# Optimization experiments

Measured on AMD Instinct MI355X. Metric: run time of the kernel, lower is better.

Reference implementation:

```python
import jax, jax.numpy as jnp
import numpy as np

H = 2048        # hidden_nodes
T = 8192        # timeseries length
WASHOUT = 200
SPECTRAL_RADIUS = 0.9


def setup_inputs() -> dict:
    key = jax.random.key(0)
    k1, k2, k3 = jax.random.split(key, 3)
    u = jax.random.normal(k1, (T,), dtype=jnp.float32)
    # w_res ~ uniform(-0.5, 0.5), rescaled to approximate spectral radius 0.9
    w_res = jax.random.uniform(k2, (H, H), dtype=jnp.float32) - 0.5
    unif_std = 1.0 / np.sqrt(12.0)
    w_res = w_res * np.float32(SPECTRAL_RADIUS / (unif_std * np.sqrt(H)))
    # w_in ~ uniform(-0.5, 0.5) * input_scaling(=1.0)
    w_in = jax.random.uniform(k3, (H,), dtype=jnp.float32) - 0.5
    w_out = jnp.ones((H,), dtype=jnp.float32)
    # w_out_density = 1.0 -> mask covers all nodes (identity gather)
    w_out_mask = jnp.arange(H, dtype=jnp.int32)
    return {"u": u, "w_res": w_res, "w_in": w_in, "w_out": w_out,
            "w_out_mask": w_out_mask, "washout": WASHOUT}


def reference(u, w_res, w_in, w_out, w_out_mask, washout):
    # Inference path (y=None, awgn_test_std=0, adc_quantization=None):
    #   x_{t} = tanh(w_in * u_t + w_res @ x_{t-1}); X[t] = x_t[mask]
    #   return X[washout:] @ w_out
    def step(x, u_t):
        x = jnp.tanh(w_in * u_t + w_res @ x)   # [H]
        return x, x[w_out_mask]                # carry, per-step readout row

    x0 = jnp.zeros((w_res.shape[0],), dtype=u.dtype)
    _, X = jax.lax.scan(step, x0, u)           # X: [T, output_dim]
    return X[washout:] @ w_out                 # [T - washout]
```

## Files before the change

### kernel.cpp

```cpp
#include <hip/hip_runtime.h>
#include <math.h>


#define H_   2048
#define RPB  8
#define NBLK 256
typedef unsigned long long ull;

__global__ void esn_zero(float* __restrict__ p, int n)
{
    int i = blockIdx.x * blockDim.x + threadIdx.x;
    int stride = gridDim.x * blockDim.x;
    for (; i < n; i += stride) p[i] = 0.0f;
}

__global__ __launch_bounds__(1024) void esn_scatter_c(const int* __restrict__ mask,
                                                      const float* __restrict__ w_out,
                                                      float* __restrict__ ws_f, int H)
{
    float* c = ws_f + 8192;
    for (int i = threadIdx.x; i < H; i += blockDim.x)
        atomicAdd(&c[mask[i]], w_out[i]);
}

__global__ __launch_bounds__(256) void esn_run(const float* __restrict__ u,
                                               const float* __restrict__ w_res,
                                               const float* __restrict__ w_in,
                                               float* __restrict__ out,
                                               float* __restrict__ ws_f,
                                               int T, int washout, int use_part)
{
    __shared__ float Wlds[RPB * H_];
    __shared__ float xs[H_];
    __shared__ float psum[4];

    const int tid  = threadIdx.x;
    const int wave = tid >> 6;
    const int lane = tid & 63;
    const int bid  = blockIdx.x;
    const int r0 = 2 * wave;
    const int grow0 = bid * RPB + r0;

    {
        const float4* src = (const float4*)(w_res + (size_t)bid * RPB * H_);
        float4* dst = (float4*)Wlds;
        for (int i = tid; i < RPB * H_ / 4; i += 256) dst[i] = src[i];
    }
    float win_l = 0.f, c_l = 0.f;
    if (lane < 2) {
        win_l = w_in[grow0 + lane];
        c_l   = ws_f[8192 + grow0 + lane];
    }

    ull* pairs = (ull*)ws_f;
    float* part = ws_f + 10240;

    const float4* w0p = (const float4*)(Wlds + (r0)     * H_);
    const float4* w1p = (const float4*)(Wlds + (r0 + 1) * H_);
    const float4* xs4 = (const float4*)xs;

    float u_next = u[0];
    __syncthreads();

    for (int k = 0; k < T; ++k) {
        const ull* sp = pairs + (k & 1) * H_;
        ull*       dp = pairs + ((k + 1) & 1) * H_;
        float uk = u_next;
        if (k + 1 < T) u_next = u[k + 1];

        ull pv[8];
#pragma unroll
        for (int i = 0; i < 8; ++i)
            pv[i] = __hip_atomic_load(sp + (i << 8) + tid, __ATOMIC_RELAXED,
                                      __HIP_MEMORY_SCOPE_AGENT);

        float4 a0 = {0.f,0.f,0.f,0.f}, a1 = {0.f,0.f,0.f,0.f};
#pragma unroll
        for (int c = 0; c < 8; ++c) {
            int spins = 0;
            while ((unsigned)(pv[c] >> 32) != (unsigned)k) {
                pv[c] = __hip_atomic_load(sp + (c << 8) + tid, __ATOMIC_RELAXED,
                                          __HIP_MEMORY_SCOPE_AGENT);
                if (++spins > 2000000) break;
            }
            xs[(c << 8) + tid] = __uint_as_float((unsigned)pv[c]);
            __syncthreads();
            float4 xv  = xs4[(c << 6) + lane];
            float4 wv0 = w0p[(c << 6) + lane];
            float4 wv1 = w1p[(c << 6) + lane];
            a0.x = fmaf(wv0.x, xv.x, a0.x); a0.y = fmaf(wv0.y, xv.y, a0.y);
            a0.z = fmaf(wv0.z, xv.z, a0.z); a0.w = fmaf(wv0.w, xv.w, a0.w);
            a1.x = fmaf(wv1.x, xv.x, a1.x); a1.y = fmaf(wv1.y, xv.y, a1.y);
            a1.z = fmaf(wv1.z, xv.z, a1.z); a1.w = fmaf(wv1.w, xv.w, a1.w);
        }
        float s0 = (a0.x + a0.y) + (a0.z + a0.w);
        float s1 = (a1.x + a1.y) + (a1.z + a1.w);
#pragma unroll
        for (int d = 1; d < 64; d <<= 1) {
            s0 += __shfl_xor(s0, d);
            s1 += __shfl_xor(s1, d);
        }

        if (lane < 2) {
            float z = fmaf(win_l, uk, (lane == 0) ? s0 : s1);
            z = fminf(fmaxf(z, -15.f), 15.f);
            float e = __expf(2.f * z);
            float t = (e - 1.f) / (e + 1.f);
            ull p = ((ull)(unsigned)(k + 1) << 32) | (ull)__float_as_uint(t);
            (void)__hip_atomic_exchange(dp + grow0 + lane, p, __ATOMIC_RELAXED,
                                        __HIP_MEMORY_SCOPE_AGENT);
            float pr = c_l * t;
            pr += __shfl_xor(pr, 1);
            if (lane == 0) psum[wave] = pr;
        }
        __syncthreads();

        if (tid == 0) {
            float pw = (psum[0] + psum[1]) + (psum[2] + psum[3]);
            if (use_part) part[(size_t)k * NBLK + bid] = pw;
            else if (k >= washout) atomicAdd(&out[k - washout], pw);
        }
    }
}

__global__ __launch_bounds__(256) void esn_reduce(const float* __restrict__ part,
                                                  float* __restrict__ out,
                                                  int out_size, int washout)
{
    int wv = threadIdx.x >> 6, lane = threadIdx.x & 63;
    int t = blockIdx.x * 4 + wv;
    if (t >= out_size) return;
    const float4* p = (const float4*)(part + (size_t)(t + washout) * NBLK);
    float4 v = p[lane];
    float s = (v.x + v.y) + (v.z + v.w);
#pragma unroll
    for (int d = 1; d < 64; d <<= 1) s += __shfl_xor(s, d);
    if (lane == 0) out[t] = s;
}

extern "C" void kernel_launch(void* const* d_in, const int* in_sizes, int n_in,
                              void* d_out, int out_size, void* d_ws, size_t ws_size,
                              hipStream_t stream)
{
    const float* u     = (const float*)d_in[0];
    const float* w_res = (const float*)d_in[1];
    const float* w_in  = (const float*)d_in[2];
    const float* w_out = (const float*)d_in[3];
    const int*   mask  = (const int*)d_in[4];
    int T = in_sizes[0];
    int H = in_sizes[2];
    int washout = T - out_size;
    float* out  = (float*)d_out;
    float* ws_f = (float*)d_ws;

    size_t need = (size_t)(10240 + (size_t)T * NBLK) * 4;
    int use_part = (ws_size >= need) ? 1 : 0;

    hipLaunchKernelGGL(esn_zero, dim3(64), dim3(256), 0, stream, ws_f, 10240);
    if (!use_part)
        hipLaunchKernelGGL(esn_zero, dim3(32), dim3(256), 0, stream, out, out_size);
    hipLaunchKernelGGL(esn_scatter_c, dim3(1), dim3(1024), 0, stream, mask, w_out, ws_f, H);

    void* args[] = { (void*)&u, (void*)&w_res, (void*)&w_in, (void*)&out,
                     (void*)&ws_f, (void*)&T, (void*)&washout, (void*)&use_part };
    hipError_t e = hipLaunchCooperativeKernel((const void*)esn_run,
                                              dim3(NBLK), dim3(256),
                                              args, 0, stream);
    if (e != hipSuccess) {
        hipLaunchKernelGGL(esn_run, dim3(NBLK), dim3(256), 0, stream,
                           u, w_res, w_in, out, ws_f, T, washout, use_part);
    }
    if (use_part)
        hipLaunchKernelGGL(esn_reduce, dim3((out_size + 3) / 4), dim3(256), 0, stream,
                           ws_f + 10240, out, out_size, washout);
}
```

Baseline: 38.02 ms.

## Split matvec by columns per wave, drop per-chunk block barriers, batch spin polls

Each wave now owns a 512-column slice of x and computes partial dot products for all 8 rows of the block, reading x straight from the polled registers instead of staging it in shared memory. This removes the eight __syncthreads per timestep that followed each chunk, leaving a single barrier to combine the per-wave partials through a double-buffered shared array. The spin wait now polls all eight chunks together with two outstanding loads per chunk, and the published value uses an atomic store instead of an exchange. In exchange, each wave does eight cross-lane reductions instead of two, and one wave handles the tanh, the publish and the readout.

Measured after the change: 42.77 ms. 12.5% more time.

```diff
diff --git a/kernel.cpp b/kernel.cpp
--- a/kernel.cpp
+++ b/kernel.cpp
@@ -31,15 +31,14 @@
                                                int T, int washout, int use_part)
 {
     __shared__ float Wlds[RPB * H_];
-    __shared__ float xs[H_];
-    __shared__ float psum[4];
+    __shared__ float psum[2][4][RPB];
 
     const int tid  = threadIdx.x;
     const int wave = tid >> 6;
     const int lane = tid & 63;
     const int bid  = blockIdx.x;
-    const int r0 = 2 * wave;
-    const int grow0 = bid * RPB + r0;
+    const int grow = bid * RPB;
+    const int jbase = (wave << 9) + lane;
 
     {
         const float4* src = (const float4*)(w_res + (size_t)bid * RPB * H_);
@@ -47,78 +46,97 @@
         for (int i = tid; i < RPB * H_ / 4; i += 256) dst[i] = src[i];
     }
     float win_l = 0.f, c_l = 0.f;
-    if (lane < 2) {
-        win_l = w_in[grow0 + lane];
-        c_l   = ws_f[8192 + grow0 + lane];
+    if (wave == 0 && lane < RPB) {
+        win_l = w_in[grow + lane];
+        c_l   = ws_f[8192 + grow + lane];
     }
 
     ull* pairs = (ull*)ws_f;
     float* part = ws_f + 10240;
 
-    const float4* w0p = (const float4*)(Wlds + (r0)     * H_);
-    const float4* w1p = (const float4*)(Wlds + (r0 + 1) * H_);
-    const float4* xs4 = (const float4*)xs;
-
     float u_next = u[0];
     __syncthreads();
 
     for (int k = 0; k < T; ++k) {
-        const ull* sp = pairs + (k & 1) * H_;
+        const ull* sp = pairs + (k & 1) * H_ + jbase;
         ull*       dp = pairs + ((k + 1) & 1) * H_;
         float uk = u_next;
         if (k + 1 < T) u_next = u[k + 1];
 
-        ull pv[8];
+        ull a[8], b[8];
 #pragma unroll
-        for (int i = 0; i < 8; ++i)
-            pv[i] = __hip_atomic_load(sp + (i << 8) + tid, __ATOMIC_RELAXED,
-                                      __HIP_MEMORY_SCOPE_AGENT);
+        for (int c = 0; c < 8; ++c)
+            a[c] = __hip_atomic_load(sp + (c << 6), __ATOMIC_RELAXED,
+                                     __HIP_MEMORY_SCOPE_AGENT);
+#pragma unroll
+        for (int c = 0; c < 8; ++c)
+            b[c] = __hip_atomic_load(sp + (c << 6), __ATOMIC_RELAXED,
+                                     __HIP_MEMORY_SCOPE_AGENT);
+        {
+            int spins = 0;
+            for (;;) {
+                unsigned stale = 0;
+#pragma unroll
+                for (int c = 0; c < 8; ++c) {
+                    if ((unsigned)(a[c] >> 32) != (unsigned)k) {
+                        a[c] = b[c];
+                        b[c] = __hip_atomic_load(sp + (c << 6), __ATOMIC_RELAXED,
+                                                 __HIP_MEMORY_SCOPE_AGENT);
+                        stale = 1;
+                    }
+                }
+                if (!stale) break;
+                if (++spins > 1000000) break;
+            }
+        }
 
         float4 a0 = {0.f,0.f,0.f,0.f}, a1 = {0.f,0.f,0.f,0.f};
 #pragma unroll
         for (int c = 0; c < 8; ++c) {
-            int spins = 0;
-            while ((unsigned)(pv[c] >> 32) != (unsigned)k) {
-                pv[c] = __hip_atomic_load(sp + (c << 8) + tid, __ATOMIC_RELAXED,
-                                          __HIP_MEMORY_SCOPE_AGENT);
-                if (++spins > 2000000) break;
-            }
-            xs[(c << 8) + tid] = __uint_as_float((unsigned)pv[c]);
-            __syncthreads();
-            float4 xv  = xs4[(c << 6) + lane];
-            float4 wv0 = w0p[(c << 6) + lane];
-            float4 wv1 = w1p[(c << 6) + lane];
-            a0.x = fmaf(wv0.x, xv.x, a0.x); a0.y = fmaf(wv0.y, xv.y, a0.y);
-            a0.z = fmaf(wv0.z, xv.z, a0.z); a0.w = fmaf(wv0.w, xv.w, a0.w);
-            a1.x = fmaf(wv1.x, xv.x, a1.x); a1.y = fmaf(wv1.y, xv.y, a1.y);
-            a1.z = fmaf(wv1.z, xv.z, a1.z); a1.w = fmaf(wv1.w, xv.w, a1.w);
+            float xv = __uint_as_float((unsigned)a[c]);
+            const float* wp = Wlds + (c << 6) + jbase;
+            a0.x = fmaf(wp[0 * H_], xv, a0.x);
+            a0.y = fmaf(wp[1 * H_], xv, a0.y);
+            a0.z = fmaf(wp[2 * H_], xv, a0.z);
+            a0.w = fmaf(wp[3 * H_], xv, a0.w);
+            a1.x = fmaf(wp[4 * H_], xv, a1.x);
+            a1.y = fmaf(wp[5 * H_], xv, a1.y);
+            a1.z = fmaf(wp[6 * H_], xv, a1.z);
+            a1.w = fmaf(wp[7 * H_], xv, a1.w);
         }
-        float s0 = (a0.x + a0.y) + (a0.z + a0.w);
-        float s1 = (a1.x + a1.y) + (a1.z + a1.w);
 #pragma unroll
         for (int d = 1; d < 64; d <<= 1) {
-            s0 += __shfl_xor(s0, d);
-            s1 += __shfl_xor(s1, d);
+            a0.x += __shfl_xor(a0.x, d); a0.y += __shfl_xor(a0.y, d);
+            a0.z += __shfl_xor(a0.z, d); a0.w += __shfl_xor(a0.w, d);
+            a1.x += __shfl_xor(a1.x, d); a1.y += __shfl_xor(a1.y, d);
+            a1.z += __shfl_xor(a1.z, d); a1.w += __shfl_xor(a1.w, d);
         }
+        if (lane == 0) {
+            float* ps = psum[k & 1][wave];
+            ps[0] = a0.x; ps[1] = a0.y; ps[2] = a0.z; ps[3] = a0.w;
+            ps[4] = a1.x; ps[5] = a1.y; ps[6] = a1.z; ps[7] = a1.w;
+        }
+        __syncthreads();
 
-        if (lane < 2) {
-            float z = fmaf(win_l, uk, (lane == 0) ? s0 : s1);
+        if (wave == 0 && lane < RPB) {
+            const int p = k & 1;
+            float z = (psum[p][0][lane] + psum[p][1][lane]) +
+                      (psum[p][2][lane] + psum[p][3][lane]);
+            z = fmaf(win_l, uk, z);
             z = fminf(fmaxf(z, -15.f), 15.f);
             float e = __expf(2.f * z);
             float t = (e - 1.f) / (e + 1.f);
-            ull p = ((ull)(unsigned)(k + 1) << 32) | (ull)__float_as_uint(t);
-            (void)__hip_atomic_exchange(dp + grow0 + lane, p, __ATOMIC_RELAXED,
-                                        __HIP_MEMORY_SCOPE_AGENT);
-            float pr = c_l * t;
-            pr += __shfl_xor(pr, 1);
-            if (lane == 0) psum[wave] = pr;
-        }
-        __syncthreads();
-
-        if (tid == 0) {
-            float pw = (psum[0] + psum[1]) + (psum[2] + psum[3]);
-            if (use_part) part[(size_t)k * NBLK + bid] = pw;
-            else if (k >= washout) atomicAdd(&out[k - washout], pw);
+            ull pr = ((ull)(unsigned)(k + 1) << 32) | (ull)__float_as_uint(t);
+            __hip_atomic_store(dp + grow + lane, pr, __ATOMIC_RELAXED,
+                               __HIP_MEMORY_SCOPE_AGENT);
+            float po = c_l * t;
+            po += __shfl_xor(po, 1);
+            po += __shfl_xor(po, 2);
+            po += __shfl_xor(po, 4);
+            if (lane == 0) {
+                if (use_part) part[(size_t)k * NBLK + bid] = po;
+                else if (k >= washout) atomicAdd(&out[k - washout], po);
+            }
         }
     }
 }
```

## Poll all state chunks together and drop per-chunk and epilogue barriers

Applied to the files above, without the earlier changes.

Each thread now issues two rounds of relaxed atomic loads for all eight chunks of the previous state and keeps polling only the stale ones. When all chunks are fresh it writes them to LDS behind a single raw s_barrier, replacing the eight __syncthreads calls that followed each chunk's spin. The per-block partial sum no longer goes through a shared psum and a trailing __syncthreads. Each wave atomically adds its two-row contribution into the partial buffer, which now has to be zeroed by an extra launch. This cuts barrier count per timestep on the serial recurrence path, at the cost of more atomic traffic and a larger zeroing pass.

New measurement: 34.35 ms. 1.11x faster.

```diff
diff --git a/kernel.cpp b/kernel.cpp
--- a/kernel.cpp
+++ b/kernel.cpp
@@ -32,14 +32,13 @@
 {
     __shared__ float Wlds[RPB * H_];
     __shared__ float xs[H_];
-    __shared__ float psum[4];
 
     const int tid  = threadIdx.x;
     const int wave = tid >> 6;
     const int lane = tid & 63;
     const int bid  = blockIdx.x;
     const int r0 = 2 * wave;
-    const int grow0 = bid * RPB + r0;
+    const int myrow = bid * RPB + r0;
 
     {
         const float4* src = (const float4*)(w_res + (size_t)bid * RPB * H_);
@@ -48,8 +47,8 @@
     }
     float win_l = 0.f, c_l = 0.f;
     if (lane < 2) {
-        win_l = w_in[grow0 + lane];
-        c_l   = ws_f[8192 + grow0 + lane];
+        win_l = w_in[myrow + lane];
+        c_l   = ws_f[8192 + myrow + lane];
     }
 
     ull* pairs = (ull*)ws_f;
@@ -68,23 +67,41 @@
         float uk = u_next;
         if (k + 1 < T) u_next = u[k + 1];
 
-        ull pv[8];
+        ull a[8], b[8];
 #pragma unroll
         for (int i = 0; i < 8; ++i)
-            pv[i] = __hip_atomic_load(sp + (i << 8) + tid, __ATOMIC_RELAXED,
-                                      __HIP_MEMORY_SCOPE_AGENT);
+            a[i] = __hip_atomic_load(sp + (i << 8) + tid, __ATOMIC_RELAXED,
+                                     __HIP_MEMORY_SCOPE_AGENT);
+#pragma unroll
+        for (int i = 0; i < 8; ++i)
+            b[i] = __hip_atomic_load(sp + (i << 8) + tid, __ATOMIC_RELAXED,
+                                     __HIP_MEMORY_SCOPE_AGENT);
+        {
+            int spins = 0;
+            for (;;) {
+                unsigned stale = 0;
+#pragma unroll
+                for (int i = 0; i < 8; ++i) {
+                    if ((unsigned)(a[i] >> 32) != (unsigned)k) {
+                        a[i] = b[i];
+                        b[i] = __hip_atomic_load(sp + (i << 8) + tid,
+                                                 __ATOMIC_RELAXED,
+                                                 __HIP_MEMORY_SCOPE_AGENT);
+                        stale = 1;
+                    }
+                }
+                if (!stale) break;
+                if (++spins > 1000000) break;
+            }
+        }
+#pragma unroll
+        for (int i = 0; i < 8; ++i)
+            xs[(i << 8) + tid] = __uint_as_float((unsigned)a[i]);
+        asm volatile("s_waitcnt lgkmcnt(0)\n\ts_barrier" ::: "memory");
 
         float4 a0 = {0.f,0.f,0.f,0.f}, a1 = {0.f,0.f,0.f,0.f};
 #pragma unroll
         for (int c = 0; c < 8; ++c) {
-            int spins = 0;
-            while ((unsigned)(pv[c] >> 32) != (unsigned)k) {
-                pv[c] = __hip_atomic_load(sp + (c << 8) + tid, __ATOMIC_RELAXED,
-                                          __HIP_MEMORY_SCOPE_AGENT);
-                if (++spins > 2000000) break;
-            }
-            xs[(c << 8) + tid] = __uint_as_float((unsigned)pv[c]);
-            __syncthreads();
             float4 xv  = xs4[(c << 6) + lane];
             float4 wv0 = w0p[(c << 6) + lane];
             float4 wv1 = w1p[(c << 6) + lane];
@@ -106,19 +123,15 @@
             z = fminf(fmaxf(z, -15.f), 15.f);
             float e = __expf(2.f * z);
             float t = (e - 1.f) / (e + 1.f);
-            ull p = ((ull)(unsigned)(k + 1) << 32) | (ull)__float_as_uint(t);
-            (void)__hip_atomic_exchange(dp + grow0 + lane, p, __ATOMIC_RELAXED,
+            ull pr = ((ull)(unsigned)(k + 1) << 32) | (ull)__float_as_uint(t);
+            (void)__hip_atomic_exchange(dp + myrow + lane, pr, __ATOMIC_RELAXED,
                                         __HIP_MEMORY_SCOPE_AGENT);
-            float pr = c_l * t;
-            pr += __shfl_xor(pr, 1);
-            if (lane == 0) psum[wave] = pr;
-        }
-        __syncthreads();
-
-        if (tid == 0) {
-            float pw = (psum[0] + psum[1]) + (psum[2] + psum[3]);
-            if (use_part) part[(size_t)k * NBLK + bid] = pw;
-            else if (k >= washout) atomicAdd(&out[k - washout], pw);
+            float po = c_l * t;
+            po += __shfl_xor(po, 1);
+            if (lane == 0 && k >= washout) {
+                if (use_part) atomicAdd(&part[(size_t)k * NBLK + bid], po);
+                else          atomicAdd(&out[k - washout], po);
+            }
         }
     }
 }
@@ -157,7 +170,10 @@
     int use_part = (ws_size >= need) ? 1 : 0;
 
     hipLaunchKernelGGL(esn_zero, dim3(64), dim3(256), 0, stream, ws_f, 10240);
-    if (!use_part)
+    if (use_part)
+        hipLaunchKernelGGL(esn_zero, dim3(256), dim3(256), 0, stream,
+                           ws_f + 10240, T * NBLK);
+    else
         hipLaunchKernelGGL(esn_zero, dim3(32), dim3(256), 0, stream, out, out_size);
     hipLaunchKernelGGL(esn_scatter_c, dim3(1), dim3(1024), 0, stream, mask, w_out, ws_f, H);
 
```
